# Kernel tuning notes

Measured on AMD Instinct MI355X. Metric: run time of the kernel, lower is better.

The kernel has to match this reference:

```python
import jax, jax.numpy as jnp
import numpy as np

K = 5            # carafe kernel size
CK = 3           # content conv kernel size = max(3, K-2)
EMB = 64         # embedding size
FILTERS = 128    # output filters


def conv1x1(x, w, b=None):
    y = jnp.einsum('bhwc,co->bhwo', x, w)
    return y if b is None else y + b


def conv_same(x, w, b):
    y = jax.lax.conv_general_dilated(x, w, (1, 1), 'SAME',
                                     dimension_numbers=('NHWC', 'HWIO', 'NHWC'))
    return y + b


def up2(x):
    return jnp.repeat(jnp.repeat(x, 2, axis=1), 2, axis=2)


def setup_inputs() -> dict:
    key = jax.random.key(0)
    ks = jax.random.split(key, 12)
    B, H, W, Cf = 2, 128, 128, 128
    h, w, Cc = 64, 64, 128
    s = 0.05
    return {
        'fine': jax.random.normal(ks[0], (B, H, W, Cf), jnp.float32),
        'coarse': jax.random.normal(ks[1], (B, h, w, Cc), jnp.float32),
        # gate 1x1 conv (Cc -> 1)
        'w_gate': jax.random.normal(ks[2], (Cc, 1), jnp.float32) * s,
        'b_gate': jnp.zeros((1,), jnp.float32),
        # SemiShift: fine 1x1 (no bias), coarse 1x1 (bias), shared content conv (EMB -> K*K)
        'w_sfine': jax.random.normal(ks[3], (Cf, EMB), jnp.float32) * s,
        'w_scoarse': jax.random.normal(ks[4], (Cc, EMB), jnp.float32) * s,
        'b_scoarse': jnp.zeros((EMB,), jnp.float32),
        'w_content': jax.random.normal(ks[5], (CK, CK, EMB, K * K), jnp.float32) * s,
        'b_content': jnp.zeros((K * K,), jnp.float32),
        # output 1x1 convs
        'w_coarse': jax.random.normal(ks[6], (Cc, FILTERS), jnp.float32) * s,
        'b_coarse': jnp.zeros((FILTERS,), jnp.float32),
        'w_fineout': jax.random.normal(ks[7], (FILTERS, FILTERS), jnp.float32) * s,
        'b_fineout': jnp.zeros((FILTERS,), jnp.float32),
    }


def reference(fine, coarse, w_gate, b_gate, w_sfine, w_scoarse, b_scoarse,
              w_content, b_content, w_coarse, b_coarse, w_fineout, b_fineout):
    B, h, w, Cc = coarse.shape
    H, W = fine.shape[1], fine.shape[2]

    # gate branch
    gate = jax.nn.sigmoid(conv1x1(coarse, w_gate, b_gate))
    gate = up2(gate)  # [B,H,W,1]

    # SemiShift kernel prediction
    f = conv1x1(fine, w_sfine)                     # no bias
    f = conv_same(f, w_content, b_content)         # [B,H,W,K*K]
    c = conv1x1(coarse, w_scoarse, b_scoarse)
    c = conv_same(c, w_content, b_content)         # [B,h,w,K*K]
    kernel = jax.nn.softmax(f + up2(c), axis=-1)   # [B,H,W,K*K]

    # CarafeConvolution: extract_patches (TF layout: [pos, ch] innermost) + NN up + grouped matmul
    p = K // 2
    xp = jnp.pad(coarse, ((0, 0), (p, p), (p, p), (0, 0)))
    patches = jnp.stack([xp[:, r:r + h, cc:cc + w, :]
                         for r in range(K) for cc in range(K)], axis=3)  # [B,h,w,K*K,Cc]
    patches = patches.reshape(B, h, w, K * K * Cc)
    patches = up2(patches)                          # [B,H,W,K*K*Cc]
    # faithful reshape as in source (group_size=1): (B,H,W,Cc,K*K)
    feat = patches.reshape(B, H, W, Cc, K * K)
    carafe = jnp.einsum('bhwck,bhwk->bhwc', feat, kernel)  # [B,H,W,Cc]

    coarse_out = conv1x1(carafe, w_coarse, b_coarse)        # [B,H,W,FILTERS]
    fine_out = conv1x1(coarse_out, w_fineout, b_fineout)    # note: applied to coarse_out as in source
    return gate * fine_out + (1.0 - gate) * coarse_out
```

## Files before the change

### kernel.cpp

```cpp
#include <hip/hip_runtime.h>
#include <hip/hip_bf16.h>
#include <cstdint>
#include <cstddef>

#define KSZ 5
#define KK 25
#define EMB 64
#define CC 128
#define FILTERS 128

typedef __attribute__((ext_vector_type(8))) short short8;
typedef __attribute__((ext_vector_type(4))) float floatx4;

__device__ inline unsigned short f32_to_bf16(float f) {
    union { float f; unsigned u; } v; v.f = f;
    unsigned u = v.u;
    unsigned r = u + 0x7FFF + ((u >> 16) & 1);
    return (unsigned short)(r >> 16);
}

#define XS_P 136
__global__ __launch_bounds__(256) void embed_both_kernel(
        const float* __restrict__ xf, const float* __restrict__ wsf,
        const float* __restrict__ xc, const float* __restrict__ wsc,
        const float* __restrict__ bias_c,
        unsigned short* __restrict__ yf, unsigned short* __restrict__ yc,
        int nf, int nemb,
        const float* __restrict__ w_content, const float* __restrict__ w_coarse,
        const float* __restrict__ w_fineout,
        unsigned short* __restrict__ wconT, unsigned short* __restrict__ wcT,
        unsigned short* __restrict__ wfT) {
    int tid = threadIdx.x;

    if ((int)blockIdx.x >= nemb) {
        int idx = (blockIdx.x - nemb) * 256 + tid;
        if (idx < 18432) {
            int n = idx / 576, k = idx - n * 576;
            float v = (n < 25) ? w_content[k * 25 + n] : 0.0f;
            wconT[idx] = f32_to_bf16(v);
        } else if (idx < 34816) {
            int j = idx - 18432;
            int o = j >> 7, k = j & 127;
            wcT[j] = f32_to_bf16(w_coarse[k * 128 + o]);
        } else {
            int j = idx - 34816;
            int o = j >> 7, k = j & 127;
            wfT[j] = f32_to_bf16(w_fineout[k * 128 + o]);
        }
        return;
    }

    __shared__ unsigned short Ws[64 * XS_P];
    bool is_f = (int)blockIdx.x < nf;
    int blk = is_f ? blockIdx.x : (blockIdx.x - nf);
    const float* x = is_f ? xf : xc;
    const float* wsrcf = is_f ? wsf : wsc;
    const float* bias = is_f ? nullptr : bias_c;
    unsigned short* y = is_f ? yf : yc;
    size_t row0 = (size_t)blk * 64;

    for (int ci = tid; ci < 2048; ci += 256) {
        int k = ci >> 4;
        int n4 = (ci & 15) * 4;
        float4 v = *(const float4*)(wsrcf + k * 64 + n4);
        Ws[(n4 + 0) * XS_P + k] = f32_to_bf16(v.x);
        Ws[(n4 + 1) * XS_P + k] = f32_to_bf16(v.y);
        Ws[(n4 + 2) * XS_P + k] = f32_to_bf16(v.z);
        Ws[(n4 + 3) * XS_P + k] = f32_to_bf16(v.w);
    }
    __syncthreads();

    int wid = tid >> 6, lane = tid & 63;
    int lr = lane & 15, hi = lane >> 4, lk = hi * 8;

    int arow = wid * 16 + lr;
    const float* xr = x + (row0 + arow) * 128;

    floatx4 acc[4];
    #pragma unroll
    for (int ni = 0; ni < 4; ++ni)
        acc[ni] = (floatx4){0.f, 0.f, 0.f, 0.f};

    #pragma unroll
    for (int kk = 0; kk < 4; ++kk) {
        float4 a0 = *(const float4*)(xr + kk * 32 + lk);
        float4 a1 = *(const float4*)(xr + kk * 32 + lk + 4);
        unsigned short ah[8];
        ah[0] = f32_to_bf16(a0.x); ah[1] = f32_to_bf16(a0.y);
        ah[2] = f32_to_bf16(a0.z); ah[3] = f32_to_bf16(a0.w);
        ah[4] = f32_to_bf16(a1.x); ah[5] = f32_to_bf16(a1.y);
        ah[6] = f32_to_bf16(a1.z); ah[7] = f32_to_bf16(a1.w);
        short8 a = *(const short8*)ah;
        #pragma unroll
        for (int ni = 0; ni < 4; ++ni) {
            short8 bb = *(const short8*)(&Ws[(ni * 16 + lr) * XS_P + kk * 32 + lk]);
            acc[ni] = __builtin_amdgcn_mfma_f32_16x16x32_bf16(a, bb, acc[ni], 0, 0, 0);
        }
    }

    #pragma unroll
    for (int ni = 0; ni < 4; ++ni) {
        int col = ni * 16 + lr;
        float bs = bias ? bias[col] : 0.0f;
        #pragma unroll
        for (int j = 0; j < 4; ++j) {
            int row = wid * 16 + hi * 4 + j;
            y[(row0 + row) * EMB + col] = f32_to_bf16(acc[ni][j] + bs);
        }
    }
}

#define SP 72
#define SB 584
__global__ __launch_bounds__(256) void content_both_kernel(
        const unsigned short* __restrict__ embf,
        const unsigned short* __restrict__ embc,
        const unsigned short* __restrict__ wT,
        const float* __restrict__ bias,
        float* __restrict__ yf, float* __restrict__ yc,
        int nf) {
    __shared__ unsigned short Es[6 * 34 * SP];
    __shared__ unsigned short Bs[32 * SB];
    int tid = threadIdx.x;
    bool is_f = (int)blockIdx.x < nf;
    int blk = is_f ? blockIdx.x : (blockIdx.x - nf);
    const unsigned short* emb = is_f ? embf : embc;
    float* y = is_f ? yf : yc;
    int HT = is_f ? 32 : 16;
    int WT = is_f ? 4 : 2;
    int Hh = is_f ? 128 : 64;
    int Ww = is_f ? 128 : 64;

    int bx = blk % WT;
    int t = blk / WT;
    int by = t % HT;
    int b = t / HT;

    for (int ci = tid; ci < 1632; ci += 256) {
        int pi = ci >> 3, e8 = ci & 7;
        int hy = pi / 34, hx = pi - hy * 34;
        int gy = by * 4 + hy - 1, gx = bx * 32 + hx - 1;
        uint4 v = {0u, 0u, 0u, 0u};
        if (gy >= 0 && gy < Hh && gx >= 0 && gx < Ww)
            v = *(const uint4*)(emb + (((size_t)(b * Hh + gy)) * Ww + gx) * EMB + e8 * 8);
        *(uint4*)(&Es[pi * SP + e8 * 8]) = v;
    }
    for (int ci = tid; ci < 2304; ci += 256) {
        int n = ci / 72, k8 = ci - n * 72;
        *(uint4*)(&Bs[n * SB + k8 * 8]) = *(const uint4*)(wT + n * 576 + k8 * 8);
    }
    __syncthreads();

    int wid = tid >> 6, lane = tid & 63;
    int lr = lane & 15, hi = lane >> 4, lk = hi * 8;

    floatx4 acc[2][2];
    #pragma unroll
    for (int mi = 0; mi < 2; ++mi)
        #pragma unroll
        for (int ni = 0; ni < 2; ++ni)
            acc[mi][ni] = (floatx4){0.f, 0.f, 0.f, 0.f};

    #pragma unroll
    for (int tap = 0; tap < 9; ++tap) {
        int dy = tap / 3, dx = tap - dy * 3;
        #pragma unroll
        for (int ks = 0; ks < 2; ++ks) {
            short8 a[2], bb[2];
            #pragma unroll
            for (int mi = 0; mi < 2; ++mi) {
                int p = wid * 32 + mi * 16 + lr;
                int r = p >> 5, c = p & 31;
                a[mi] = *(const short8*)(&Es[((r + dy) * 34 + (c + dx)) * SP + ks * 32 + lk]);
            }
            #pragma unroll
            for (int ni = 0; ni < 2; ++ni)
                bb[ni] = *(const short8*)(&Bs[(ni * 16 + lr) * SB + tap * 64 + ks * 32 + lk]);
            #pragma unroll
            for (int mi = 0; mi < 2; ++mi)
                #pragma unroll
                for (int ni = 0; ni < 2; ++ni)
                    acc[mi][ni] = __builtin_amdgcn_mfma_f32_16x16x32_bf16(a[mi], bb[ni], acc[mi][ni], 0, 0, 0);
        }
    }

    #pragma unroll
    for (int mi = 0; mi < 2; ++mi) {
        #pragma unroll
        for (int ni = 0; ni < 2; ++ni) {
            int n = ni * 16 + lr;
            if (n < KK) {
                float bs = bias[n];
                #pragma unroll
                for (int j = 0; j < 4; ++j) {
                    int p = wid * 32 + mi * 16 + hi * 4 + j;
                    int r = p >> 5, c = p & 31;
                    size_t gq = ((size_t)(b * Hh + by * 4 + r)) * Ww + bx * 32 + c;
                    y[gq * KK + n] = acc[mi][ni][j] + bs;
                }
            }
        }
    }
}

#define LDSP 136
__global__ __launch_bounds__(256) void carafe_final_kernel(
        const float* __restrict__ coarse,
        const float* __restrict__ f_conv,
        const float* __restrict__ c_conv,
        const float* __restrict__ w_gate,
        const float* __restrict__ b_gate,
        const unsigned short* __restrict__ WcT,
        const unsigned short* __restrict__ WfT,
        const float* __restrict__ b_coarse,
        const float* __restrict__ b_fineout,
        float* __restrict__ out) {
    __shared__ __align__(16) char smem[58624];
    float* patches = (float*)smem;
    float* wsm     = (float*)(smem + 32768);
    float* g_lds   = (float*)(smem + 40960);
    unsigned short* Ws = (unsigned short*)smem;
    unsigned short* Xs = (unsigned short*)(smem + 41216);

    const int h = 64, w = 64, H2 = 128, W2 = 128;
    int tid = threadIdx.x;
    int blk = blockIdx.x;
    int cx0 = (blk & 15) * 4;
    int cy0 = ((blk >> 4) & 15) * 4;
    int b = blk >> 8;

    for (int ci = tid; ci < 2048; ci += 256) {
        int pi = ci >> 5;
        int c4 = (ci & 31) << 2;
        int sy = cy0 - 2 + (pi >> 3);
        int sx = cx0 - 2 + (pi & 7);
        float4 v = {0.f, 0.f, 0.f, 0.f};
        if (sy >= 0 && sy < h && sx >= 0 && sx < w)
            v = *(const float4*)(coarse + (((size_t)(b * h + sy)) * w + sx) * CC + c4);
        *(float4*)(&patches[pi * 128 + c4]) = v;
    }

    int wid = tid >> 6, lane = tid & 63;
    {
        int k = lane & 31;
        #pragma unroll
        for (int pass = 0; pass < 8; ++pass) {
            int fp = wid * 16 + pass * 2 + (lane >> 5);
            int fry = fp >> 3, frx = fp & 7;
            int fy = 2 * cy0 + fry, fx = 2 * cx0 + frx;
            int cy = cy0 + (fry >> 1), cx = cx0 + (frx >> 1);
            size_t fq = ((size_t)(b * H2 + fy)) * W2 + fx;
            size_t cq = ((size_t)(b * h + cy)) * w + cx;
            float v = -1e30f;
            if (k < KK)
                v = f_conv[fq * KK + k] + c_conv[cq * KK + k];
            float m = v;
            #pragma unroll
            for (int mask = 16; mask > 0; mask >>= 1)
                m = fmaxf(m, __shfl_xor(m, mask, 32));
            float e = (k < KK) ? __expf(v - m) : 0.0f;
            float s = e;
            #pragma unroll
            for (int mask = 16; mask > 0; mask >>= 1)
                s += __shfl_xor(s, mask, 32);
            wsm[fp * 32 + k] = e / s;
        }
    }
    __syncthreads();

    {
        int cp = tid >> 4;
        int part = tid & 15;
        int pidx = ((cp >> 2) + 2) * 8 + (cp & 3) + 2;
        const float* pc = patches + pidx * 128 + part * 8;
        float4 a0 = *(const float4*)(pc);
        float4 a1 = *(const float4*)(pc + 4);
        float4 g0 = *(const float4*)(w_gate + part * 8);
        float4 g1 = *(const float4*)(w_gate + part * 8 + 4);
        float acc = a0.x * g0.x + a0.y * g0.y + a0.z * g0.z + a0.w * g0.w
                  + a1.x * g1.x + a1.y * g1.y + a1.z * g1.z + a1.w * g1.w;
        #pragma unroll
        for (int mask = 8; mask > 0; mask >>= 1)
            acc += __shfl_xor(acc, mask, 16);
        if (part == 0) {
            float z = acc + b_gate[0];
            g_lds[cp] = 1.0f / (1.0f + __expf(-z));
        }
    }

    {
        int c   = tid & 127;
        int cpg = tid >> 7;
        int offs[28];
        int c25 = c * 25;
        #pragma unroll
        for (int j = 0; j < 28; ++j) {
            int i = c25 + j;
            int p = i >> 7;
            int ch = i & 127;
            int pd = (p * 205) >> 10;
            int pm = p - pd * 5;
            offs[j] = (pd * 8 + pm) * 128 + ch;
        }
        #pragma unroll
        for (int it = 0; it < 8; ++it) {
            int cp = cpg * 8 + it;
            int ry = cp >> 2, rx = cp & 3;
            int cpbase = (ry * 8 + rx) * 128;
            int fpA = (2 * ry) * 8 + 2 * rx;
            float a00 = 0.f, a01 = 0.f, a10 = 0.f, a11 = 0.f;
            #pragma unroll
            for (int j4 = 0; j4 < 7; ++j4) {
                float4 wA = *(const float4*)(&wsm[fpA * 32 + j4 * 4]);
                float4 wB = *(const float4*)(&wsm[(fpA + 1) * 32 + j4 * 4]);
                float4 wC = *(const float4*)(&wsm[(fpA + 8) * 32 + j4 * 4]);
                float4 wD = *(const float4*)(&wsm[(fpA + 9) * 32 + j4 * 4]);
                #pragma unroll
                for (int jj = 0; jj < 4; ++jj) {
                    float pv = patches[cpbase + offs[j4 * 4 + jj]];
                    float wa = (jj == 0) ? wA.x : (jj == 1) ? wA.y : (jj == 2) ? wA.z : wA.w;
                    float wb = (jj == 0) ? wB.x : (jj == 1) ? wB.y : (jj == 2) ? wB.z : wB.w;
                    float wc = (jj == 0) ? wC.x : (jj == 1) ? wC.y : (jj == 2) ? wC.z : wC.w;
                    float wd = (jj == 0) ? wD.x : (jj == 1) ? wD.y : (jj == 2) ? wD.z : wD.w;
                    a00 += wa * pv;
                    a01 += wb * pv;
                    a10 += wc * pv;
                    a11 += wd * pv;
                }
            }
            Xs[fpA * LDSP + c]       = f32_to_bf16(a00);
            Xs[(fpA + 1) * LDSP + c] = f32_to_bf16(a01);
            Xs[(fpA + 8) * LDSP + c] = f32_to_bf16(a10);
            Xs[(fpA + 9) * LDSP + c] = f32_to_bf16(a11);
        }
    }
    __syncthreads();

    {
        const uint4* wsrc = (const uint4*)WcT;
        for (int ci = tid; ci < 2048; ci += 256) {
            int r = ci >> 4, c = ci & 15;
            *(uint4*)(&Ws[r * LDSP + c * 8]) = wsrc[ci];
        }
    }
    __syncthreads();

    int wm = wid >> 1, wn = wid & 1;
    int lr = lane & 15;
    int lk = (lane >> 4) * 8;
    int lrow4 = (lane >> 4) * 4;

    floatx4 acc1[2][4];
    #pragma unroll
    for (int mi = 0; mi < 2; ++mi)
        #pragma unroll
        for (int ni = 0; ni < 4; ++ni)
            acc1[mi][ni] = (floatx4){0.f, 0.f, 0.f, 0.f};

    #pragma unroll
    for (int kk = 0; kk < 128; kk += 32) {
        short8 a[2], bb[4];
        #pragma unroll
        for (int mi = 0; mi < 2; ++mi)
            a[mi] = *(const short8*)(&Xs[(wm * 32 + mi * 16 + lr) * LDSP + kk + lk]);
        #pragma unroll
        for (int ni = 0; ni < 4; ++ni)
            bb[ni] = *(const short8*)(&Ws[(wn * 64 + ni * 16 + lr) * LDSP + kk + lk]);
        #pragma unroll
        for (int mi = 0; mi < 2; ++mi)
            #pragma unroll
            for (int ni = 0; ni < 4; ++ni)
                acc1[mi][ni] = __builtin_amdgcn_mfma_f32_16x16x32_bf16(a[mi], bb[ni], acc1[mi][ni], 0, 0, 0);
    }
    __syncthreads();

    {
        const uint4* wsrc = (const uint4*)WfT;
        for (int ci = tid; ci < 2048; ci += 256) {
            int r = ci >> 4, c = ci & 15;
            *(uint4*)(&Ws[r * LDSP + c * 8]) = wsrc[ci];
        }
    }
    #pragma unroll
    for (int mi = 0; mi < 2; ++mi) {
        #pragma unroll
        for (int ni = 0; ni < 4; ++ni) {
            int col = wn * 64 + ni * 16 + lr;
            float bc = b_coarse[col];
            #pragma unroll
            for (int j = 0; j < 4; ++j) {
                int row = wm * 32 + mi * 16 + lrow4 + j;
                float v = acc1[mi][ni][j] + bc;
                acc1[mi][ni][j] = v;
                Xs[row * LDSP + col] = f32_to_bf16(v);
            }
        }
    }
    __syncthreads();

    floatx4 acc2[2][4];
    #pragma unroll
    for (int mi = 0; mi < 2; ++mi)
        #pragma unroll
        for (int ni = 0; ni < 4; ++ni)
            acc2[mi][ni] = (floatx4){0.f, 0.f, 0.f, 0.f};

    #pragma unroll
    for (int kk = 0; kk < 128; kk += 32) {
        short8 a[2], bb[4];
        #pragma unroll
        for (int mi = 0; mi < 2; ++mi)
            a[mi] = *(const short8*)(&Xs[(wm * 32 + mi * 16 + lr) * LDSP + kk + lk]);
        #pragma unroll
        for (int ni = 0; ni < 4; ++ni)
            bb[ni] = *(const short8*)(&Ws[(wn * 64 + ni * 16 + lr) * LDSP + kk + lk]);
        #pragma unroll
        for (int mi = 0; mi < 2; ++mi)
            #pragma unroll
            for (int ni = 0; ni < 4; ++ni)
                acc2[mi][ni] = __builtin_amdgcn_mfma_f32_16x16x32_bf16(a[mi], bb[ni], acc2[mi][ni], 0, 0, 0);
    }

    #pragma unroll
    for (int mi = 0; mi < 2; ++mi) {
        #pragma unroll
        for (int ni = 0; ni < 4; ++ni) {
            int col = wn * 64 + ni * 16 + lr;
            float bf = b_fineout[col];
            #pragma unroll
            for (int j = 0; j < 4; ++j) {
                int row = wm * 32 + mi * 16 + lrow4 + j;
                int fry = row >> 3, frx = row & 7;
                float g = g_lds[((fry >> 1) << 2) + (frx >> 1)];
                int fy = 2 * cy0 + fry, fx = 2 * cx0 + frx;
                size_t q = ((size_t)(b * H2 + fy)) * W2 + fx;
                float co = acc1[mi][ni][j];
                float fo = acc2[mi][ni][j] + bf;
                out[q * FILTERS + col] = g * fo + (1.0f - g) * co;
            }
        }
    }
}

extern "C" void kernel_launch(void* const* d_in, const int* in_sizes, int n_in,
                              void* d_out, int out_size, void* d_ws, size_t ws_size,
                              hipStream_t stream) {
    const float* fine      = (const float*)d_in[0];
    const float* coarse    = (const float*)d_in[1];
    const float* w_gate    = (const float*)d_in[2];
    const float* b_gate    = (const float*)d_in[3];
    const float* w_sfine   = (const float*)d_in[4];
    const float* w_scoarse = (const float*)d_in[5];
    const float* b_scoarse = (const float*)d_in[6];
    const float* w_content = (const float*)d_in[7];
    const float* b_content = (const float*)d_in[8];
    const float* w_coarse  = (const float*)d_in[9];
    const float* b_coarse  = (const float*)d_in[10];
    const float* w_fineout = (const float*)d_in[11];
    const float* b_fineout = (const float*)d_in[12];
    float* out = (float*)d_out;

    const int B = 2, H = 128, W = 128, h = 64, w = 64;
    const int MF = B * H * W;
    const int MC = B * h * w;

    char* ws = (char*)d_ws;
    size_t off = 0;
    auto alloc = [&](size_t bytes) {
        void* p = ws + off;
        off = (off + bytes + 255) & ~(size_t)255;
        return p;
    };
    unsigned short* f_emb    = (unsigned short*)alloc((size_t)MF * EMB * 2);
    unsigned short* c_emb    = (unsigned short*)alloc((size_t)MC * EMB * 2);
    float* f_conv            = (float*)alloc((size_t)MF * KK * 4);
    float* c_conv            = (float*)alloc((size_t)MC * KK * 4);
    unsigned short* wconT    = (unsigned short*)alloc(32 * 576 * 2);
    unsigned short* wcT      = (unsigned short*)alloc(128 * 128 * 2);
    unsigned short* wfT      = (unsigned short*)alloc(128 * 128 * 2);

    const int NEF = MF / 64;
    const int NEC = MC / 64;
    const int NEB = NEF + NEC;
    const int NWT = 200;
    const int NCF = B * (H / 4) * (W / 32);
    const int NCC = B * (h / 4) * (w / 32);

    embed_both_kernel<<<NEB + NWT, 256, 0, stream>>>(fine, w_sfine, coarse, w_scoarse, b_scoarse,
                                                     f_emb, c_emb, NEF, NEB,
                                                     w_content, w_coarse, w_fineout,
                                                     wconT, wcT, wfT);
    content_both_kernel<<<NCF + NCC, 256, 0, stream>>>(f_emb, c_emb, wconT, b_content,
                                                       f_conv, c_conv, NCF);
    carafe_final_kernel<<<B * 16 * 16, 256, 0, stream>>>(coarse, f_conv, c_conv, w_gate, b_gate,
                                                         wcT, wfT, b_coarse, b_fineout, out);
}
```

Before: 47.41 us.

## Halve carafe tile height to double block count and pad conv outputs to 32

The final fused kernel now handles a 2x4 coarse tile (16x8 fine pixels... 64 fine pixels) per block instead of 4x4, which doubles the grid to 1024 blocks and cuts LDS use so more blocks fit per CU. Each warp does one MFMA row tile instead of two, and the gate computation uses half the threads. The content conv outputs are also stored with a stride of 32 floats instead of 25, so each pixel's row is aligned. The trade-off is more redundant halo loads of coarse patches and more per-block weight staging relative to the work done.

```diff
diff --git a/kernel.cpp b/kernel.cpp
--- a/kernel.cpp
+++ b/kernel.cpp
@@ -8,6 +8,7 @@
 #define EMB 64
 #define CC 128
 #define FILTERS 128
+#define CST 32
 
 typedef __attribute__((ext_vector_type(8))) short short8;
 typedef __attribute__((ext_vector_type(4))) float floatx4;
@@ -196,7 +197,7 @@
                     int p = wid * 32 + mi * 16 + hi * 4 + j;
                     int r = p >> 5, c = p & 31;
                     size_t gq = ((size_t)(b * Hh + by * 4 + r)) * Ww + bx * 32 + c;
-                    y[gq * KK + n] = acc[mi][ni][j] + bs;
+                    y[gq * CST + n] = acc[mi][ni][j] + bs;
                 }
             }
         }
@@ -215,21 +216,21 @@
         const float* __restrict__ b_coarse,
         const float* __restrict__ b_fineout,
         float* __restrict__ out) {
-    __shared__ __align__(16) char smem[58624];
+    __shared__ __align__(16) char smem[43552];
     float* patches = (float*)smem;
-    float* wsm     = (float*)(smem + 32768);
-    float* g_lds   = (float*)(smem + 40960);
+    float* wsm     = (float*)(smem + 24576);
+    float* g_lds   = (float*)(smem + 34816);
     unsigned short* Ws = (unsigned short*)smem;
-    unsigned short* Xs = (unsigned short*)(smem + 41216);
+    unsigned short* Xs = (unsigned short*)(smem + 34848);
 
     const int h = 64, w = 64, H2 = 128, W2 = 128;
     int tid = threadIdx.x;
     int blk = blockIdx.x;
     int cx0 = (blk & 15) * 4;
-    int cy0 = ((blk >> 4) & 15) * 4;
-    int b = blk >> 8;
-
-    for (int ci = tid; ci < 2048; ci += 256) {
+    int cy0 = ((blk >> 4) & 31) * 2;
+    int b = blk >> 9;
+
+    for (int ci = tid; ci < 1536; ci += 256) {
         int pi = ci >> 5;
         int c4 = (ci & 31) << 2;
         int sy = cy0 - 2 + (pi >> 3);
@@ -244,8 +245,8 @@
     {
         int k = lane & 31;
         #pragma unroll
-        for (int pass = 0; pass < 8; ++pass) {
-            int fp = wid * 16 + pass * 2 + (lane >> 5);
+        for (int pass = 0; pass < 4; ++pass) {
+            int fp = wid * 8 + pass * 2 + (lane >> 5);
             int fry = fp >> 3, frx = fp & 7;
             int fy = 2 * cy0 + fry, fx = 2 * cx0 + frx;
             int cy = cy0 + (fry >> 1), cx = cx0 + (frx >> 1);
@@ -253,7 +254,7 @@
             size_t cq = ((size_t)(b * h + cy)) * w + cx;
             float v = -1e30f;
             if (k < KK)
-                v = f_conv[fq * KK + k] + c_conv[cq * KK + k];
+                v = f_conv[fq * CST + k] + c_conv[cq * CST + k];
             float m = v;
             #pragma unroll
             for (int mask = 16; mask > 0; mask >>= 1)
@@ -268,10 +269,11 @@
     }
     __syncthreads();
 
-    {
+    if (tid < 128) {
         int cp = tid >> 4;
         int part = tid & 15;
-        int pidx = ((cp >> 2) + 2) * 8 + (cp & 3) + 2;
+        int ry = cp >> 2, rx = cp & 3;
+        int pidx = (ry + 2) * 8 + (rx + 2);
         const float* pc = patches + pidx * 128 + part * 8;
         float4 a0 = *(const float4*)(pc);
         float4 a1 = *(const float4*)(pc + 4);
@@ -303,8 +305,8 @@
             offs[j] = (pd * 8 + pm) * 128 + ch;
         }
         #pragma unroll
-        for (int it = 0; it < 8; ++it) {
-            int cp = cpg * 8 + it;
+        for (int it = 0; it < 4; ++it) {
+            int cp = cpg * 4 + it;
             int ry = cp >> 2, rx = cp & 3;
             int cpbase = (ry * 8 + rx) * 128;
             int fpA = (2 * ry) * 8 + 2 * rx;
@@ -350,27 +352,21 @@
     int lk = (lane >> 4) * 8;
     int lrow4 = (lane >> 4) * 4;
 
-    floatx4 acc1[2][4];
-    #pragma unroll
-    for (int mi = 0; mi < 2; ++mi)
-        #pragma unroll
-        for (int ni = 0; ni < 4; ++ni)
-            acc1[mi][ni] = (floatx4){0.f, 0.f, 0.f, 0.f};
+    floatx4 acc1[4];
+    #pragma unroll
+    for (int ni = 0; ni < 4; ++ni)
+        acc1[ni] = (floatx4){0.f, 0.f, 0.f, 0.f};
 
     #pragma unroll
     for (int kk = 0; kk < 128; kk += 32) {
-        short8 a[2], bb[4];
-        #pragma unroll
-        for (int mi = 0; mi < 2; ++mi)
-            a[mi] = *(const short8*)(&Xs[(wm * 32 + mi * 16 + lr) * LDSP + kk + lk]);
+        short8 a = *(const short8*)(&Xs[(wm * 16 + lr) * LDSP + kk + lk]);
+        short8 bb[4];
         #pragma unroll
         for (int ni = 0; ni < 4; ++ni)
             bb[ni] = *(const short8*)(&Ws[(wn * 64 + ni * 16 + lr) * LDSP + kk + lk]);
         #pragma unroll
-        for (int mi = 0; mi < 2; ++mi)
-            #pragma unroll
-            for (int ni = 0; ni < 4; ++ni)
-                acc1[mi][ni] = __builtin_amdgcn_mfma_f32_16x16x32_bf16(a[mi], bb[ni], acc1[mi][ni], 0, 0, 0);
+        for (int ni = 0; ni < 4; ++ni)
+            acc1[ni] = __builtin_amdgcn_mfma_f32_16x16x32_bf16(a, bb[ni], acc1[ni], 0, 0, 0);
     }
     __syncthreads();
 
@@ -382,62 +378,50 @@
         }
     }
     #pragma unroll
-    for (int mi = 0; mi < 2; ++mi) {
-        #pragma unroll
-        for (int ni = 0; ni < 4; ++ni) {
-            int col = wn * 64 + ni * 16 + lr;
-            float bc = b_coarse[col];
-            #pragma unroll
-            for (int j = 0; j < 4; ++j) {
-                int row = wm * 32 + mi * 16 + lrow4 + j;
-                float v = acc1[mi][ni][j] + bc;
-                acc1[mi][ni][j] = v;
-                Xs[row * LDSP + col] = f32_to_bf16(v);
-            }
-        }
-    }
-    __syncthreads();
-
-    floatx4 acc2[2][4];
-    #pragma unroll
-    for (int mi = 0; mi < 2; ++mi)
-        #pragma unroll
-        for (int ni = 0; ni < 4; ++ni)
-            acc2[mi][ni] = (floatx4){0.f, 0.f, 0.f, 0.f};
+    for (int ni = 0; ni < 4; ++ni) {
+        int col = wn * 64 + ni * 16 + lr;
+        float bc = b_coarse[col];
+        #pragma unroll
+        for (int j = 0; j < 4; ++j) {
+            int row = wm * 16 + lrow4 + j;
+            float v = acc1[ni][j] + bc;
+            acc1[ni][j] = v;
+            Xs[row * LDSP + col] = f32_to_bf16(v);
+        }
+    }
+    __syncthreads();
+
+    floatx4 acc2[4];
+    #pragma unroll
+    for (int ni = 0; ni < 4; ++ni)
+        acc2[ni] = (floatx4){0.f, 0.f, 0.f, 0.f};
 
     #pragma unroll
     for (int kk = 0; kk < 128; kk += 32) {
-        short8 a[2], bb[4];
-        #pragma unroll
-        for (int mi = 0; mi < 2; ++mi)
-            a[mi] = *(const short8*)(&Xs[(wm * 32 + mi * 16 + lr) * LDSP + kk + lk]);
+        short8 a = *(const short8*)(&Xs[(wm * 16 + lr) * LDSP + kk + lk]);
+        short8 bb[4];
         #pragma unroll
         for (int ni = 0; ni < 4; ++ni)
             bb[ni] = *(const short8*)(&Ws[(wn * 64 + ni * 16 + lr) * LDSP + kk + lk]);
         #pragma unroll
-        for (int mi = 0; mi < 2; ++mi)
-            #pragma unroll
-            for (int ni = 0; ni < 4; ++ni)
-                acc2[mi][ni] = __builtin_amdgcn_mfma_f32_16x16x32_bf16(a[mi], bb[ni], acc2[mi][ni], 0, 0, 0);
-    }
-
-    #pragma unroll
-    for (int mi = 0; mi < 2; ++mi) {
-        #pragma unroll
-        for (int ni = 0; ni < 4; ++ni) {
-            int col = wn * 64 + ni * 16 + lr;
-            float bf = b_fineout[col];
-            #pragma unroll
-            for (int j = 0; j < 4; ++j) {
-                int row = wm * 32 + mi * 16 + lrow4 + j;
-                int fry = row >> 3, frx = row & 7;
-                float g = g_lds[((fry >> 1) << 2) + (frx >> 1)];
-                int fy = 2 * cy0 + fry, fx = 2 * cx0 + frx;
-                size_t q = ((size_t)(b * H2 + fy)) * W2 + fx;
-                float co = acc1[mi][ni][j];
-                float fo = acc2[mi][ni][j] + bf;
-                out[q * FILTERS + col] = g * fo + (1.0f - g) * co;
-            }
+        for (int ni = 0; ni < 4; ++ni)
+            acc2[ni] = __builtin_amdgcn_mfma_f32_16x16x32_bf16(a, bb[ni], acc2[ni], 0, 0, 0);
+    }
+
+    #pragma unroll
+    for (int ni = 0; ni < 4; ++ni) {
+        int col = wn * 64 + ni * 16 + lr;
+        float bf = b_fineout[col];
+        #pragma unroll
+        for (int j = 0; j < 4; ++j) {
+            int row = wm * 16 + lrow4 + j;
+            int fry = row >> 3, frx = row & 7;
+            float g = g_lds[((fry >> 1) << 2) + (frx >> 1)];
+            int fy = 2 * cy0 + fry, fx = 2 * cx0 + frx;
+            size_t q = ((size_t)(b * H2 + fy)) * W2 + fx;
+            float co = acc1[ni][j];
+            float fo = acc2[ni][j] + bf;
+            out[q * FILTERS + col] = g * fo + (1.0f - g) * co;
         }
     }
 }
@@ -473,8 +457,8 @@
     };
     unsigned short* f_emb    = (unsigned short*)alloc((size_t)MF * EMB * 2);
     unsigned short* c_emb    = (unsigned short*)alloc((size_t)MC * EMB * 2);
-    float* f_conv            = (float*)alloc((size_t)MF * KK * 4);
-    float* c_conv            = (float*)alloc((size_t)MC * KK * 4);
+    float* f_conv            = (float*)alloc((size_t)MF * CST * 4);
+    float* c_conv            = (float*)alloc((size_t)MC * CST * 4);
     unsigned short* wconT    = (unsigned short*)alloc(32 * 576 * 2);
     unsigned short* wcT      = (unsigned short*)alloc(128 * 128 * 2);
     unsigned short* wfT      = (unsigned short*)alloc(128 * 128 * 2);
@@ -492,6 +476,6 @@
                                                      wconT, wcT, wfT);
     content_both_kernel<<<NCF + NCC, 256, 0, stream>>>(f_emb, c_emb, wconT, b_content,
                                                        f_conv, c_conv, NCF);
-    carafe_final_kernel<<<B * 16 * 16, 256, 0, stream>>>(coarse, f_conv, c_conv, w_gate, b_gate,
+    carafe_final_kernel<<<B * 32 * 16, 256, 0, stream>>>(coarse, f_conv, c_conv, w_gate, b_gate,
                                                          wcT, wfT, b_coarse, b_fineout, out);
 }
```

New measurement: 48.87 us. 1.03x slower.
